# Performance work log

Measured on AMD Instinct MI355X. Metric: run time of the kernel, lower is better.

The kernel has to match this reference:

```python
import jax, jax.numpy as jnp
import numpy as np

BN_EPS = 1e-5
N_NODES = 100000
N_EDGES = 1600000
F_IN = 128
F_HID = 256
N_ITEMS = 128


def setup_inputs() -> dict:
    key = jax.random.key(0)
    ks = jax.random.split(key, 6)
    return {
        "node_feature": jax.random.normal(ks[0], (N_NODES, F_IN), jnp.float32),
        "edge_index": jax.random.randint(ks[1], (2, N_EDGES), 0, N_NODES, jnp.int64),
        "items_ready_to_cache": jnp.arange(N_ITEMS, dtype=jnp.int64),
        "gcn_w": jax.random.normal(ks[2], (F_IN, F_HID), jnp.float32) / np.sqrt(F_IN),
        "gcn_b": jnp.zeros((F_HID,), jnp.float32),
        "bn_gamma": jnp.ones((F_HID,), jnp.float32),
        "bn_beta": jnp.zeros((F_HID,), jnp.float32),
        "emb_table": jax.random.normal(ks[3], (F_IN, F_IN), jnp.float32),
        "proj_w": jax.random.normal(ks[4], (F_HID, F_IN), jnp.float32) / np.sqrt(F_HID),
        "proj_b": jnp.zeros((F_IN,), jnp.float32),
    }


def _gcn_conv(x, edge_index, w, b, n_nodes):
    # PyG GCNConv: add self-loops, symmetric normalization, scatter-add to target.
    loop = jnp.arange(n_nodes, dtype=edge_index.dtype)
    src = jnp.concatenate([edge_index[0], loop])
    dst = jnp.concatenate([edge_index[1], loop])
    h = x @ w                                  # [N, F_HID]
    deg = jax.ops.segment_sum(jnp.ones_like(dst, dtype=h.dtype), dst,
                              num_segments=n_nodes)
    dinv = jnp.where(deg > 0, jax.lax.rsqrt(deg), 0.0)
    norm = dinv[src] * dinv[dst]               # [E+N]
    msgs = h[src] * norm[:, None]              # gather + scale  [E+N, F_HID]
    out = jax.ops.segment_sum(msgs, dst, num_segments=n_nodes)  # scatter-add
    return out + b


def reference(node_feature, edge_index, items_ready_to_cache, gcn_w, gcn_b,
              bn_gamma, bn_beta, emb_table, proj_w, proj_b):
    n_nodes = node_feature.shape[0]
    x = _gcn_conv(node_feature, edge_index, gcn_w, gcn_b, n_nodes)
    # BatchNorm1d in training mode: batch stats (biased variance)
    mean = jnp.mean(x, axis=0)
    var = jnp.mean((x - mean) ** 2, axis=0)
    x = bn_gamma * (x - mean) * jax.lax.rsqrt(var + BN_EPS) + bn_beta
    x = jax.nn.relu(x)
    rsu_embedding = x[0:1] @ proj_w + proj_b   # [1, F_IN]
    # item_id_to_index collapses indices to arange(len(items))
    n_items = items_ready_to_cache.shape[0]
    items_embeddings = emb_table[jnp.arange(n_items)]  # [n_items, F_IN]
    scores = items_embeddings @ rsu_embedding[0]       # [n_items]
    return scores, rsu_embedding
```

## Files before the change

### kernel.cpp

```cpp
#include <hip/hip_runtime.h>
#include <hip/hip_bf16.h>


#define THREADS 256

__global__ __launch_bounds__(THREADS) void deg_rank_kernel(const int* __restrict__ ei,
                                                           int* __restrict__ deg,
                                                           int* __restrict__ rank,
                                                           int E, int N) {
    int e = blockIdx.x * THREADS + threadIdx.x;
    if (e < E) {
        unsigned d = (unsigned)ei[E + e];
        int p = 0;
        if (d < (unsigned)N) p = atomicAdd(&deg[d], 1);
        rank[e] = p;
    }
}

__global__ __launch_bounds__(THREADS) void scan1_kernel(const int* __restrict__ deg,
                                                        int* __restrict__ rowptr,
                                                        int* __restrict__ bsum,
                                                        float* __restrict__ dinv, int n) {
    __shared__ int sh[THREADS];
    const int t = threadIdx.x, b = blockIdx.x;
    const int base = b * 1024 + t * 4;
    int v0 = (base + 0 < n) ? deg[base + 0] : 0;
    int v1 = (base + 1 < n) ? deg[base + 1] : 0;
    int v2 = (base + 2 < n) ? deg[base + 2] : 0;
    int v3 = (base + 3 < n) ? deg[base + 3] : 0;
    if (base + 0 < n) dinv[base + 0] = rsqrtf((float)(v0 + 1));
    if (base + 1 < n) dinv[base + 1] = rsqrtf((float)(v1 + 1));
    if (base + 2 < n) dinv[base + 2] = rsqrtf((float)(v2 + 1));
    if (base + 3 < n) dinv[base + 3] = rsqrtf((float)(v3 + 1));
    const int local = v0 + v1 + v2 + v3;
    sh[t] = local;
    __syncthreads();
    int run = local;
    for (int off = 1; off < THREADS; off <<= 1) {
        int add = (t >= off) ? sh[t - off] : 0;
        __syncthreads();
        run += add;
        sh[t] = run;
        __syncthreads();
    }
    const int excl = run - local;
    if (base + 0 < n) rowptr[base + 0] = excl;
    if (base + 1 < n) rowptr[base + 1] = excl + v0;
    if (base + 2 < n) rowptr[base + 2] = excl + v0 + v1;
    if (base + 3 < n) rowptr[base + 3] = excl + v0 + v1 + v2;
    if (t == 0) bsum[b] = sh[THREADS - 1];
}

__global__ __launch_bounds__(THREADS) void scan2_kernel(const int* __restrict__ bsum,
                                                        int* __restrict__ boff, int nb,
                                                        float* __restrict__ colsumS,
                                                        float* __restrict__ G,
                                                        int* __restrict__ workctr) {
    __shared__ int sh[THREADS];
    const int t = threadIdx.x;
    const int local = (t < nb) ? bsum[t] : 0;
    sh[t] = local;
    __syncthreads();
    int run = local;
    for (int off = 1; off < THREADS; off <<= 1) {
        int add = (t >= off) ? sh[t - off] : 0;
        __syncthreads();
        run += add;
        sh[t] = run;
        __syncthreads();
    }
    boff[t] = run - local;
    if (t < 128) colsumS[t] = 0.f;
    if (t == 0) *workctr = 0;
    for (int u = t; u < 16384; u += THREADS) G[u] = 0.f;
}

__global__ __launch_bounds__(THREADS) void scatter_kernel(const int* __restrict__ ei,
                                                          const int* __restrict__ rowptr,
                                                          const int* __restrict__ boff,
                                                          const int* __restrict__ rank,
                                                          int* __restrict__ csr,
                                                          int E, int N) {
    int e = blockIdx.x * THREADS + threadIdx.x;
    if (e < E) {
        unsigned d = (unsigned)ei[E + e];
        if (d < (unsigned)N) {
            int base = rowptr[d] + boff[d >> 10] + rank[e];
            if ((unsigned)base < (unsigned)E) csr[base] = ei[e];
        }
    }
}

__global__ __launch_bounds__(512) void agg_syrk_kernel(
        const float* __restrict__ x, const int* __restrict__ rowptr,
        const int* __restrict__ boff, const int* __restrict__ csr,
        const float* __restrict__ dinv, int* __restrict__ workctr,
        float* __restrict__ Gpart, float* __restrict__ colsumS,
        float* __restrict__ agg0, int n, int E, int NC) {
    __shared__ float Asm[64 * 132];
    __shared__ int sh_c;
    const int t = threadIdx.x;
    const int lane = t & 63, wv = t >> 6;
    const int p0 = (t >> 5) * 8;
    const int q0 = (t & 31) * 4;
    const float* xl = x + lane * 2;

    float acc[8][4];
#pragma unroll
    for (int i = 0; i < 8; ++i)
#pragma unroll
        for (int j = 0; j < 4; ++j) acc[i][j] = 0.f;
    float s_acc = 0.f;

    for (;;) {
        if (t == 0) sh_c = atomicAdd(workctr, 1);
        __syncthreads();
        const int c = sh_c;
        if (c >= NC) break;

        for (int rr = 0; rr < 8; ++rr) {
            const int r = wv * 8 + rr;
            const int i = c * 64 + r;
            float ax = 0.f, ay = 0.f;
            if (i < n) {
                const int e0 = rowptr[i] + boff[i >> 10];
                const int e1 = (i + 1 < n) ? rowptr[i + 1] + boff[(i + 1) >> 10] : E;
                const float di = dinv[i];
                const float2 xs = *(const float2*)(xl + (size_t)i * 128);
                ax = di * xs.x; ay = di * xs.y;
                int e = e0;
                for (; e + 8 <= e1; e += 8) {
                    int ss[8]; float ww[8]; float2 pv[8];
#pragma unroll
                    for (int u = 0; u < 8; ++u) {
                        int s = csr[e + u];
                        ss[u] = ((unsigned)s < (unsigned)n) ? s : 0;
                    }
#pragma unroll
                    for (int u = 0; u < 8; ++u) ww[u] = dinv[ss[u]];
#pragma unroll
                    for (int u = 0; u < 8; ++u)
                        pv[u] = *(const float2*)(xl + (size_t)ss[u] * 128);
#pragma unroll
                    for (int u = 0; u < 8; ++u) {
                        ax = fmaf(ww[u], pv[u].x, ax);
                        ay = fmaf(ww[u], pv[u].y, ay);
                    }
                }
                for (; e < e1; ++e) {
                    int s = csr[e];
                    s = ((unsigned)s < (unsigned)n) ? s : 0;
                    float w = dinv[s];
                    float2 p = *(const float2*)(xl + (size_t)s * 128);
                    ax = fmaf(w, p.x, ax);
                    ay = fmaf(w, p.y, ay);
                }
                ax *= di; ay *= di;
            }
            *(float2*)(Asm + r * 132 + lane * 2) = make_float2(ax, ay);
        }
        __syncthreads();

        if (c == 0 && t < 32)
            *(float4*)(agg0 + t * 4) = *(const float4*)(Asm + t * 4);

#pragma unroll 4
        for (int r = 0; r < 64; ++r) {
            const float* row = Asm + r * 132;
            float4 a0 = *(const float4*)(row + p0);
            float4 a1 = *(const float4*)(row + p0 + 4);
            float4 bq = *(const float4*)(row + q0);
            float ap[8] = {a0.x, a0.y, a0.z, a0.w, a1.x, a1.y, a1.z, a1.w};
            float aq[4] = {bq.x, bq.y, bq.z, bq.w};
#pragma unroll
            for (int pp = 0; pp < 8; ++pp)
#pragma unroll
                for (int qq = 0; qq < 4; ++qq)
                    acc[pp][qq] = fmaf(ap[pp], aq[qq], acc[pp][qq]);
        }
        if (t < 128) {
            float sa = 0.f;
            for (int r = 0; r < 64; ++r) sa += Asm[r * 132 + t];
            s_acc += sa;
        }
        __syncthreads();
    }

    float* gp = Gpart + (size_t)blockIdx.x * 16384;
#pragma unroll
    for (int pp = 0; pp < 8; ++pp)
        *(float4*)(gp + (p0 + pp) * 128 + q0) =
            make_float4(acc[pp][0], acc[pp][1], acc[pp][2], acc[pp][3]);
    if (t < 128) atomicAdd(&colsumS[t], s_acc);
}

__global__ __launch_bounds__(THREADS) void greduce_kernel(const float* __restrict__ Gpart,
                                                          float* __restrict__ G, int NB) {
    const int seg = blockIdx.x >> 4;
    const int i4 = (blockIdx.x & 15) * THREADS + threadIdx.x;
    const int b0 = (seg * NB) / 8, b1 = ((seg + 1) * NB) / 8;
    float4 a = make_float4(0.f, 0.f, 0.f, 0.f);
    for (int b = b0; b < b1; ++b) {
        float4 v = *(const float4*)(Gpart + (size_t)b * 16384 + i4 * 4);
        a.x += v.x; a.y += v.y; a.z += v.z; a.w += v.w;
    }
    atomicAdd(&G[i4 * 4 + 0], a.x);
    atomicAdd(&G[i4 * 4 + 1], a.y);
    atomicAdd(&G[i4 * 4 + 2], a.z);
    atomicAdd(&G[i4 * 4 + 3], a.w);
}

__global__ __launch_bounds__(THREADS) void stats_kernel(
        const float* __restrict__ G, const float* __restrict__ W,
        const float* __restrict__ bias, const float* __restrict__ colsumS,
        const float* __restrict__ agg0, float* __restrict__ colsum,
        float* __restrict__ colsumsq, float* __restrict__ row0, int n) {
    __shared__ float wsm[128];
    __shared__ float red[THREADS], red2[THREADS], red3[THREADS];
    const int t = threadIdx.x, j = blockIdx.x;
    if (t < 128) wsm[t] = W[t * 256 + j];
    __syncthreads();
    float part = 0.f;
    const float wq = wsm[t & 127];
    const int pbase = t >> 7;
#pragma unroll 8
    for (int u = 0; u < 64; ++u)
        part = fmaf(G[u * 256 + t], wsm[pbase + u * 2], part);
    red[t] = part * wq;
    red2[t] = (t < 128) ? colsumS[t] * wsm[t] : 0.f;
    red3[t] = (t < 128) ? agg0[t] * wsm[t] : 0.f;
    __syncthreads();
    for (int s = 128; s > 0; s >>= 1) {
        if (t < s) { red[t] += red[t + s]; red2[t] += red2[t + s]; red3[t] += red3[t + s]; }
        __syncthreads();
    }
    if (t == 0) {
        const float b = bias[j];
        const float sw = red2[0];
        colsum[j]   = sw + (float)n * b;
        colsumsq[j] = red[0] + 2.f * b * sw + (float)n * b * b;
        row0[j]     = red3[0] + b;
    }
}

__global__ __launch_bounds__(THREADS) void finalize_kernel(
        const float* __restrict__ colsum, const float* __restrict__ colsumsq,
        const float* __restrict__ row0, const float* __restrict__ gamma,
        const float* __restrict__ beta, const float* __restrict__ proj_w,
        const float* __restrict__ proj_b, const float* __restrict__ emb,
        float* __restrict__ out, int n_nodes, int n_items) {
    __shared__ float x0[256];
    __shared__ float rsu[128];
    const int t = threadIdx.x;
    const float invn = 1.0f / (float)n_nodes;
    {
        float mean = colsum[t] * invn;
        float var = colsumsq[t] * invn - mean * mean;
        float r = rsqrtf(var + 1e-5f);
        float v = gamma[t] * (row0[t] - mean) * r + beta[t];
        x0[t] = v > 0.f ? v : 0.f;
    }
    __syncthreads();
    if (t < 128) {
        float sacc = proj_b[t];
        for (int c = 0; c < 256; ++c) sacc = fmaf(x0[c], proj_w[c * 128 + t], sacc);
        rsu[t] = sacc;
        out[128 + t] = sacc;
    }
    __syncthreads();
    if (t < n_items) {
        float sacc = 0.f;
        for (int j = 0; j < 128; ++j) sacc = fmaf(emb[t * 128 + j], rsu[j], sacc);
        out[t] = sacc;
    }
}

extern "C" void kernel_launch(void* const* d_in, const int* in_sizes, int n_in,
                              void* d_out, int out_size, void* d_ws, size_t ws_size,
                              hipStream_t stream) {
    const float* node_feature = (const float*)d_in[0];
    const int*   edge_index   = (const int*)d_in[1];
    const float* gcn_w  = (const float*)d_in[3];
    const float* gcn_b  = (const float*)d_in[4];
    const float* bn_g   = (const float*)d_in[5];
    const float* bn_b   = (const float*)d_in[6];
    const float* emb    = (const float*)d_in[7];
    const float* proj_w = (const float*)d_in[8];
    const float* proj_b = (const float*)d_in[9];
    float* out = (float*)d_out;

    const int N = in_sizes[0] / 128;
    const int E = in_sizes[1] / 2;
    const int n_items = in_sizes[2];

    char* base = (char*)d_ws;
    size_t off = 0;
    auto alloc = [&](size_t bytes) -> void* {
        void* p = (void*)(base + off);
        off += (bytes + 255) & ~(size_t)255;
        return p;
    };
    int*   deg      = (int*)alloc((size_t)N * 4);
    int*   rank     = (int*)alloc((size_t)E * 4);
    int*   rowptr   = (int*)alloc((size_t)N * 4);
    int*   bsum     = (int*)alloc(256 * 4);
    int*   boff     = (int*)alloc(256 * 4);
    float* dinv     = (float*)alloc((size_t)N * 4);
    int*   csr      = (int*)alloc((size_t)E * 4);
    float* colsumS  = (float*)alloc(128 * 4);
    float* agg0     = (float*)alloc(128 * 4);
    float* G        = (float*)alloc(16384 * 4);
    float* colsum   = (float*)alloc(256 * 4);
    float* colsumsq = (float*)alloc(256 * 4);
    float* row0     = (float*)alloc(256 * 4);
    int*   workctr  = (int*)alloc(256);
    int NB = (int)((ws_size > off) ? ((ws_size - off) / (16384 * 4)) : 0);
    if (NB > 512) NB = 512;
    if (NB < 8) NB = 8;
    float* Gpart    = (float*)alloc((size_t)NB * 16384 * 4);

    const int nbE = (E + THREADS - 1) / THREADS;
    const int nchunks = (N + 1023) >> 10;
    const int NC = (N + 63) / 64;

    hipMemsetAsync(deg, 0, (size_t)N * 4, stream);

    deg_rank_kernel<<<nbE, THREADS, 0, stream>>>(edge_index, deg, rank, E, N);
    scan1_kernel<<<nchunks, THREADS, 0, stream>>>(deg, rowptr, bsum, dinv, N);
    scan2_kernel<<<1, THREADS, 0, stream>>>(bsum, boff, nchunks, colsumS, G, workctr);
    scatter_kernel<<<nbE, THREADS, 0, stream>>>(edge_index, rowptr, boff, rank, csr, E, N);
    agg_syrk_kernel<<<NB, 512, 0, stream>>>(node_feature, rowptr, boff, csr, dinv,
                                            workctr, Gpart, colsumS, agg0, N, E, NC);
    greduce_kernel<<<128, THREADS, 0, stream>>>(Gpart, G, NB);
    stats_kernel<<<256, THREADS, 0, stream>>>(G, gcn_w, gcn_b, colsumS, agg0,
                                              colsum, colsumsq, row0, N);
    finalize_kernel<<<1, THREADS, 0, stream>>>(colsum, colsumsq, row0, bn_g, bn_b,
                                               proj_w, proj_b, emb, out, N, n_items);
}
```

Baseline: 421.7 us.

## Vectorize edge preprocessing kernels and shrink aggregation chunk to 32 rows

Deg/rank and scatter kernels now process four edges per thread with int4 loads. The fused aggregation+Gram kernel processes 32-row chunks instead of 64 and the cap on persistent blocks is raised to 1024. This aims to improve load balance and memory-level parallelism. In exchange it adds more per-chunk synchronisation and a larger partial-Gram reduction.

```diff
diff --git a/kernel.cpp b/kernel.cpp
--- a/kernel.cpp
+++ b/kernel.cpp
@@ -3,17 +3,26 @@
 
 
 #define THREADS 256
+#define CHUNK 32
 
 __global__ __launch_bounds__(THREADS) void deg_rank_kernel(const int* __restrict__ ei,
                                                            int* __restrict__ deg,
                                                            int* __restrict__ rank,
                                                            int E, int N) {
-    int e = blockIdx.x * THREADS + threadIdx.x;
-    if (e < E) {
-        unsigned d = (unsigned)ei[E + e];
-        int p = 0;
-        if (d < (unsigned)N) p = atomicAdd(&deg[d], 1);
-        rank[e] = p;
+    int e4 = (blockIdx.x * THREADS + threadIdx.x) * 4;
+    if (e4 + 3 < E) {
+        int4 d = *(const int4*)(ei + E + e4);
+        int4 r;
+        r.x = ((unsigned)d.x < (unsigned)N) ? atomicAdd(&deg[d.x], 1) : 0;
+        r.y = ((unsigned)d.y < (unsigned)N) ? atomicAdd(&deg[d.y], 1) : 0;
+        r.z = ((unsigned)d.z < (unsigned)N) ? atomicAdd(&deg[d.z], 1) : 0;
+        r.w = ((unsigned)d.w < (unsigned)N) ? atomicAdd(&deg[d.w], 1) : 0;
+        *(int4*)(rank + e4) = r;
+    } else if (e4 < E) {
+        for (int u = e4; u < E; ++u) {
+            unsigned d = (unsigned)ei[E + u];
+            rank[u] = (d < (unsigned)N) ? atomicAdd(&deg[d], 1) : 0;
+        }
     }
 }
 
@@ -81,12 +90,34 @@
                                                           const int* __restrict__ rank,
                                                           int* __restrict__ csr,
                                                           int E, int N) {
-    int e = blockIdx.x * THREADS + threadIdx.x;
-    if (e < E) {
-        unsigned d = (unsigned)ei[E + e];
-        if (d < (unsigned)N) {
-            int base = rowptr[d] + boff[d >> 10] + rank[e];
-            if ((unsigned)base < (unsigned)E) csr[base] = ei[e];
+    int e4 = (blockIdx.x * THREADS + threadIdx.x) * 4;
+    if (e4 + 3 < E) {
+        int4 d = *(const int4*)(ei + E + e4);
+        int4 s = *(const int4*)(ei + e4);
+        int4 r = *(const int4*)(rank + e4);
+        if ((unsigned)d.x < (unsigned)N) {
+            int p = rowptr[d.x] + boff[d.x >> 10] + r.x;
+            if ((unsigned)p < (unsigned)E) csr[p] = s.x;
+        }
+        if ((unsigned)d.y < (unsigned)N) {
+            int p = rowptr[d.y] + boff[d.y >> 10] + r.y;
+            if ((unsigned)p < (unsigned)E) csr[p] = s.y;
+        }
+        if ((unsigned)d.z < (unsigned)N) {
+            int p = rowptr[d.z] + boff[d.z >> 10] + r.z;
+            if ((unsigned)p < (unsigned)E) csr[p] = s.z;
+        }
+        if ((unsigned)d.w < (unsigned)N) {
+            int p = rowptr[d.w] + boff[d.w >> 10] + r.w;
+            if ((unsigned)p < (unsigned)E) csr[p] = s.w;
+        }
+    } else if (e4 < E) {
+        for (int u = e4; u < E; ++u) {
+            unsigned d = (unsigned)ei[E + u];
+            if (d < (unsigned)N) {
+                int p = rowptr[d] + boff[d >> 10] + rank[u];
+                if ((unsigned)p < (unsigned)E) csr[p] = ei[u];
+            }
         }
     }
 }
@@ -97,7 +128,7 @@
         const float* __restrict__ dinv, int* __restrict__ workctr,
         float* __restrict__ Gpart, float* __restrict__ colsumS,
         float* __restrict__ agg0, int n, int E, int NC) {
-    __shared__ float Asm[64 * 132];
+    __shared__ float Asm[CHUNK * 132];
     __shared__ int sh_c;
     const int t = threadIdx.x;
     const int lane = t & 63, wv = t >> 6;
@@ -118,9 +149,9 @@
         const int c = sh_c;
         if (c >= NC) break;
 
-        for (int rr = 0; rr < 8; ++rr) {
-            const int r = wv * 8 + rr;
-            const int i = c * 64 + r;
+        for (int rr = 0; rr < CHUNK / 8; ++rr) {
+            const int r = wv * (CHUNK / 8) + rr;
+            const int i = c * CHUNK + r;
             float ax = 0.f, ay = 0.f;
             if (i < n) {
                 const int e0 = rowptr[i] + boff[i >> 10];
@@ -165,7 +196,7 @@
             *(float4*)(agg0 + t * 4) = *(const float4*)(Asm + t * 4);
 
 #pragma unroll 4
-        for (int r = 0; r < 64; ++r) {
+        for (int r = 0; r < CHUNK; ++r) {
             const float* row = Asm + r * 132;
             float4 a0 = *(const float4*)(row + p0);
             float4 a1 = *(const float4*)(row + p0 + 4);
@@ -180,7 +211,8 @@
         }
         if (t < 128) {
             float sa = 0.f;
-            for (int r = 0; r < 64; ++r) sa += Asm[r * 132 + t];
+#pragma unroll 4
+            for (int r = 0; r < CHUNK; ++r) sa += Asm[r * 132 + t];
             s_acc += sa;
         }
         __syncthreads();
@@ -315,20 +347,20 @@
     float* row0     = (float*)alloc(256 * 4);
     int*   workctr  = (int*)alloc(256);
     int NB = (int)((ws_size > off) ? ((ws_size - off) / (16384 * 4)) : 0);
-    if (NB > 512) NB = 512;
+    if (NB > 1024) NB = 1024;
     if (NB < 8) NB = 8;
     float* Gpart    = (float*)alloc((size_t)NB * 16384 * 4);
 
-    const int nbE = (E + THREADS - 1) / THREADS;
+    const int nbE4 = (E / 4 + THREADS - 1) / THREADS;
     const int nchunks = (N + 1023) >> 10;
-    const int NC = (N + 63) / 64;
+    const int NC = (N + CHUNK - 1) / CHUNK;
 
     hipMemsetAsync(deg, 0, (size_t)N * 4, stream);
 
-    deg_rank_kernel<<<nbE, THREADS, 0, stream>>>(edge_index, deg, rank, E, N);
+    deg_rank_kernel<<<nbE4, THREADS, 0, stream>>>(edge_index, deg, rank, E, N);
     scan1_kernel<<<nchunks, THREADS, 0, stream>>>(deg, rowptr, bsum, dinv, N);
     scan2_kernel<<<1, THREADS, 0, stream>>>(bsum, boff, nchunks, colsumS, G, workctr);
-    scatter_kernel<<<nbE, THREADS, 0, stream>>>(edge_index, rowptr, boff, rank, csr, E, N);
+    scatter_kernel<<<nbE4, THREADS, 0, stream>>>(edge_index, rowptr, boff, rank, csr, E, N);
     agg_syrk_kernel<<<NB, 512, 0, stream>>>(node_feature, rowptr, boff, csr, dinv,
                                             workctr, Gpart, colsumS, agg0, N, E, NC);
     greduce_kernel<<<128, THREADS, 0, stream>>>(Gpart, G, NB);
```

Measured after the change: 443.6 us. +5.2%, slower.
